# Kernel tuning notes

Hardware: AMD Instinct MI355X
Metric: run time of the kernel (lower is better)

Reference implementation:

```python
import jax, jax.numpy as jnp
import numpy as np

N_NODES = 50000
N_EDGES = 600000
N_PAIRS = 200000
D_IN, D_HID = 128, 256


def _sage_conv(x, src, dst, W_l, b_l, W_r, num_nodes):
    # PyG SAGEConv('mean'): out = mean_agg(x_j) @ W_l + b_l + x @ W_r
    msgs = x[src]                                              # [E, d] gather
    agg = jax.ops.segment_sum(msgs, dst, num_segments=num_nodes)
    deg = jax.ops.segment_sum(jnp.ones((src.shape[0],), x.dtype), dst,
                              num_segments=num_nodes)
    agg = agg / jnp.maximum(deg, 1.0)[:, None]                 # mean, safe for deg=0
    return agg @ W_l + b_l + x @ W_r


def setup_inputs() -> dict:
    key = jax.random.key(0)
    ks = jax.random.split(key, 8)
    s = lambda d: 1.0 / np.sqrt(d)
    return {
        "features": jax.random.normal(ks[0], (N_NODES, D_IN), jnp.float32),
        "edge_index": jax.random.randint(ks[1], (2, N_EDGES), 0, N_NODES, jnp.int64),
        "mask": jax.random.randint(ks[2], (N_PAIRS, 2), 0, N_NODES, jnp.int64),
        "W1l": jax.random.normal(ks[3], (D_IN, D_HID), jnp.float32) * s(D_IN),
        "b1l": jnp.zeros((D_HID,), jnp.float32),
        "W1r": jax.random.normal(ks[4], (D_IN, D_HID), jnp.float32) * s(D_IN),
        "W2l": jax.random.normal(ks[5], (D_HID, D_IN), jnp.float32) * s(D_HID),
        "b2l": jnp.zeros((D_IN,), jnp.float32),
        "W2r": jax.random.normal(ks[6], (D_HID, D_IN), jnp.float32) * s(D_HID),
        "Wlin": jax.random.normal(ks[7], (2 * D_IN, 1), jnp.float32) * s(2 * D_IN),
        "blin": jnp.zeros((1,), jnp.float32),
    }


def reference(features, edge_index, mask, W1l, b1l, W1r, W2l, b2l, W2r, Wlin, blin):
    n = features.shape[0]
    src, dst = edge_index[0], edge_index[1]
    h = _sage_conv(features, src, dst, W1l, b1l, W1r, n)       # [N, 256]
    h = jax.nn.relu(h)                                         # dropout p=0 -> identity
    h = _sage_conv(h, src, dst, W2l, b2l, W2r, n)              # [N, 128]
    m = mask.T                                                 # [2, P]
    p1 = jax.lax.stop_gradient(h[m[0]])                        # detach in original
    p2 = jax.lax.stop_gradient(h[m[1]])
    pair = jnp.concatenate((p1, p2), axis=1)                   # [P, 256]
    return jax.nn.sigmoid(pair @ Wlin + blin)                  # [P, 1]
```

## Files before the change

kernel.cpp:

```cpp
#include <hip/hip_runtime.h>
#include <math.h>

#define NN 50000
#define NE 600000
#define NP 200000
#define NB_SCAN 49

typedef unsigned int uint;
typedef unsigned short ushort;
typedef __attribute__((ext_vector_type(8))) short bf16x8;
typedef __attribute__((ext_vector_type(4))) float f32x4;

__device__ __forceinline__ ushort f2bf(float f) {
    uint u = __float_as_uint(f);
    uint r = (u + 0x7FFFu + ((u >> 16) & 1u)) >> 16;
    return (ushort)r;
}
__device__ __forceinline__ float bf2f(uint lo16) {
    return __uint_as_float(lo16 << 16);
}

__device__ __forceinline__ int wave_iscan(int v, int lane) {
#pragma unroll
    for (int off = 1; off < 64; off <<= 1) {
        int t = __shfl_up(v, off, 64);
        if (lane >= off) v += t;
    }
    return v;
}

template <int K, int N>
__device__ __forceinline__ void prepB_one(int idx, const float* __restrict__ Wt,
                                          const float* __restrict__ Wb,
                                          ushort* __restrict__ Bp) {
    int lane = idx & 63;
    int nt = (idx >> 6) % (N / 16);
    int ct = idx / (64 * (N / 16));
    int n = nt * 16 + (lane & 15);
    int kb = ct * 32 + (lane >> 4) * 8;
#pragma unroll
    for (int j = 0; j < 8; j++) {
        int k = kb + j;
        float w = (k < K / 2) ? Wt[(size_t)k * N + n] : Wb[(size_t)(k - K / 2) * N + n];
        Bp[(size_t)idx * 8 + j] = f2bf(w);
    }
}

#define T_PREP (NN * 32)
#define T_DEG  (T_PREP + NE)
#define T_B1   (T_DEG + 8192)
#define T_PQ   (T_B1 + 1024)
#define T_CAB  (T_PQ + 2)
__global__ void k_pre(const float* __restrict__ x, uint* __restrict__ A1u,
                      const int* __restrict__ dst, int* __restrict__ deg,
                      const float* __restrict__ W1l, const float* __restrict__ W1r,
                      ushort* __restrict__ Bp1,
                      const float* __restrict__ W2l, const float* __restrict__ W2r,
                      const float* __restrict__ Wlin, const float* __restrict__ b2l,
                      float* __restrict__ pq, float* __restrict__ cab) {
    int t = blockIdx.x * 256 + threadIdx.x;
    if (t < T_PREP) {
        int n = t >> 5, c4 = t & 31;
        float4 v = *(const float4*)(x + (size_t)n * 128 + c4 * 4);
        uint2 o;
        o.x = (uint)f2bf(v.x) | ((uint)f2bf(v.y) << 16);
        o.y = (uint)f2bf(v.z) | ((uint)f2bf(v.w) << 16);
        *(uint2*)(A1u + (size_t)n * 128 + 64 + c4 * 2) = o;
    } else if (t < T_DEG) {
        atomicAdd(deg + dst[t - T_PREP], 1);
    } else if (t < T_B1) {
        prepB_one<256, 256>(t - T_DEG, W1l, W1r, Bp1);
    } else if (t < T_PQ) {
        int idx = t - T_B1;
        int vec = idx >> 8;
        int k = idx & 255;
        const float* W = (vec < 2) ? W2l : W2r;
        const float* wl = Wlin + (vec & 1) * 128;
        float s = 0.f;
#pragma unroll 4
        for (int j = 0; j < 128; j++) s += W[(size_t)k * 128 + j] * wl[j];
        pq[idx] = s;
    } else if (t < T_CAB) {
        int i = t - T_PQ;
        float s = 0.f;
        for (int j = 0; j < 128; j++) s += b2l[j] * Wlin[i * 128 + j];
        cab[i] = s;
    }
}

__global__ __launch_bounds__(1024) void k_scan1(const int* __restrict__ deg,
                                                int* __restrict__ excl,
                                                int* __restrict__ bsum) {
    int tid = threadIdx.x;
    int i = blockIdx.x * 1024 + tid;
    int lane = tid & 63, wid = tid >> 6;
    int v = (i < NN) ? deg[i] : 0;
    int incl = wave_iscan(v, lane);
    __shared__ int wt[16];
    if (lane == 63) wt[wid] = incl;
    __syncthreads();
    if (tid < 16) {
        int w = wt[tid];
#pragma unroll
        for (int off = 1; off < 16; off <<= 1) {
            int t = __shfl_up(w, off, 64);
            if (tid >= off) w += t;
        }
        wt[tid] = w;
    }
    __syncthreads();
    int base = (wid > 0) ? wt[wid - 1] : 0;
    if (i < NN) excl[i] = incl - v + base;
    if (tid == 0) bsum[blockIdx.x] = wt[15];
}

__global__ __launch_bounds__(1024) void k_scan23(const int* __restrict__ excl,
                                                 const int* __restrict__ bsum,
                                                 int* __restrict__ rowptr,
                                                 int* __restrict__ cursor) {
    __shared__ int boff;
    int tid = threadIdx.x;
    if (tid < 64) {
        int v = (tid < NB_SCAN) ? bsum[tid] : 0;
        int incl = wave_iscan(v, tid);
        if (tid == (int)blockIdx.x) boff = incl - v;
    }
    __syncthreads();
    int i = blockIdx.x * 1024 + tid;
    if (i < NN) {
        int v = excl[i] + boff;
        rowptr[i] = v;
        cursor[i] = v;
    }
    if (i == 0) rowptr[NN] = NE;
}

__global__ void k_fill(const int* __restrict__ src, const int* __restrict__ dst,
                       int* __restrict__ cursor, int* __restrict__ ssrc) {
    int e = blockIdx.x * 256 + threadIdx.x;
    if (e >= NE) return;
    int d = dst[e];
    int pos = atomicAdd(cursor + d, 1);
    ssrc[pos] = src[e];
}

__global__ void k_agg1(uint* __restrict__ A1u, const int* __restrict__ rowptr,
                       const int* __restrict__ ssrc) {
    int t = blockIdx.x * 256 + threadIdx.x;
    int n = t >> 6;
    if (n >= NN) return;
    int lane = t & 63;
    int g = lane >> 4;
    int s = lane & 15;
    int r0 = rowptr[n], r1 = rowptr[n + 1];
    float a0[8] = {0.f, 0.f, 0.f, 0.f, 0.f, 0.f, 0.f, 0.f};
    float a1[8] = {0.f, 0.f, 0.f, 0.f, 0.f, 0.f, 0.f, 0.f};
    int e = r0;
    for (; e + 8 <= r1; e += 8) {
        int sA = ssrc[e + g];
        int sB = ssrc[e + 4 + g];
        uint4 vA = *(const uint4*)(A1u + (size_t)sA * 128 + 64 + s * 4);
        uint4 vB = *(const uint4*)(A1u + (size_t)sB * 128 + 64 + s * 4);
        a0[0] += bf2f(vA.x & 0xffffu); a0[1] += bf2f(vA.x >> 16);
        a0[2] += bf2f(vA.y & 0xffffu); a0[3] += bf2f(vA.y >> 16);
        a0[4] += bf2f(vA.z & 0xffffu); a0[5] += bf2f(vA.z >> 16);
        a0[6] += bf2f(vA.w & 0xffffu); a0[7] += bf2f(vA.w >> 16);
        a1[0] += bf2f(vB.x & 0xffffu); a1[1] += bf2f(vB.x >> 16);
        a1[2] += bf2f(vB.y & 0xffffu); a1[3] += bf2f(vB.y >> 16);
        a1[4] += bf2f(vB.z & 0xffffu); a1[5] += bf2f(vB.z >> 16);
        a1[6] += bf2f(vB.w & 0xffffu); a1[7] += bf2f(vB.w >> 16);
    }
    if (e + 4 <= r1) {
        int sA = ssrc[e + g];
        uint4 vA = *(const uint4*)(A1u + (size_t)sA * 128 + 64 + s * 4);
        a0[0] += bf2f(vA.x & 0xffffu); a0[1] += bf2f(vA.x >> 16);
        a0[2] += bf2f(vA.y & 0xffffu); a0[3] += bf2f(vA.y >> 16);
        a0[4] += bf2f(vA.z & 0xffffu); a0[5] += bf2f(vA.z >> 16);
        a0[6] += bf2f(vA.w & 0xffffu); a0[7] += bf2f(vA.w >> 16);
        e += 4;
    }
    int rem = r1 - e;
    if (g < rem) {
        int sB = ssrc[e + g];
        uint4 vB = *(const uint4*)(A1u + (size_t)sB * 128 + 64 + s * 4);
        a1[0] += bf2f(vB.x & 0xffffu); a1[1] += bf2f(vB.x >> 16);
        a1[2] += bf2f(vB.y & 0xffffu); a1[3] += bf2f(vB.y >> 16);
        a1[4] += bf2f(vB.z & 0xffffu); a1[5] += bf2f(vB.z >> 16);
        a1[6] += bf2f(vB.w & 0xffffu); a1[7] += bf2f(vB.w >> 16);
    }
    float ax[8];
#pragma unroll
    for (int j = 0; j < 8; j++) ax[j] = a0[j] + a1[j];
#pragma unroll
    for (int j = 0; j < 8; j++) {
        ax[j] += __shfl_xor(ax[j], 16, 64);
        ax[j] += __shfl_xor(ax[j], 32, 64);
    }
    if (g == 0) {
        float sc = 1.0f / fmaxf((float)(r1 - r0), 1.0f);
        uint4 o;
        o.x = (uint)f2bf(ax[0] * sc) | ((uint)f2bf(ax[1] * sc) << 16);
        o.y = (uint)f2bf(ax[2] * sc) | ((uint)f2bf(ax[3] * sc) << 16);
        o.z = (uint)f2bf(ax[4] * sc) | ((uint)f2bf(ax[5] * sc) << 16);
        o.w = (uint)f2bf(ax[6] * sc) | ((uint)f2bf(ax[7] * sc) << 16);
        *(uint4*)(A1u + (size_t)n * 128 + s * 4) = o;
    }
}

__global__ __launch_bounds__(256) void k_gemm1(const ushort* __restrict__ A,
                                               const ushort* __restrict__ Bp,
                                               const float* __restrict__ bias,
                                               const float* __restrict__ pq,
                                               float2* __restrict__ g2,
                                               float2* __restrict__ u2) {
    const int K = 256, NTW = 4;
    int wave = threadIdx.x >> 6;
    int lane = threadIdx.x & 63;
    int quad = lane >> 4;
    int l15 = lane & 15;
    int mbase = blockIdx.x * 32;
    int r0 = mbase + l15;       if (r0 >= NN) r0 = NN - 1;
    int r1 = mbase + 16 + l15;  if (r1 >= NN) r1 = NN - 1;
    f32x4 acc0[NTW], acc1[NTW];
#pragma unroll
    for (int i = 0; i < NTW; i++) {
        acc0[i] = (f32x4){0.f, 0.f, 0.f, 0.f};
        acc1[i] = (f32x4){0.f, 0.f, 0.f, 0.f};
    }
    const bf16x8* bp = (const bf16x8*)Bp;
#pragma unroll
    for (int ct = 0; ct < K / 32; ct++) {
        bf16x8 a0 = *(const bf16x8*)(A + (size_t)r0 * K + ct * 32 + quad * 8);
        bf16x8 a1 = *(const bf16x8*)(A + (size_t)r1 * K + ct * 32 + quad * 8);
#pragma unroll
        for (int ntl = 0; ntl < NTW; ntl++) {
            int nt = wave * NTW + ntl;
            bf16x8 b = bp[(ct * 16 + nt) * 64 + lane];
            acc0[ntl] = __builtin_amdgcn_mfma_f32_16x16x32_bf16(a0, b, acc0[ntl], 0, 0, 0);
            acc1[ntl] = __builtin_amdgcn_mfma_f32_16x16x32_bf16(a1, b, acc1[ntl], 0, 0, 0);
        }
    }
    float pga[2][4] = {{0,0,0,0},{0,0,0,0}}, pgb[2][4] = {{0,0,0,0},{0,0,0,0}};
    float pua[2][4] = {{0,0,0,0},{0,0,0,0}}, pub[2][4] = {{0,0,0,0},{0,0,0,0}};
#pragma unroll
    for (int ntl = 0; ntl < NTW; ntl++) {
        int col = (wave * NTW + ntl) * 16 + l15;
        float bv = bias[col];
        float wpa = pq[col], wpb = pq[256 + col];
        float wqa = pq[512 + col], wqb = pq[768 + col];
#pragma unroll
        for (int reg = 0; reg < 4; reg++) {
            float v0 = acc0[ntl][reg] + bv;  v0 = v0 > 0.f ? v0 : 0.f;
            float v1 = acc1[ntl][reg] + bv;  v1 = v1 > 0.f ? v1 : 0.f;
            pga[0][reg] += v0 * wpa;  pgb[0][reg] += v0 * wpb;
            pua[0][reg] += v0 * wqa;  pub[0][reg] += v0 * wqb;
            pga[1][reg] += v1 * wpa;  pgb[1][reg] += v1 * wpb;
            pua[1][reg] += v1 * wqa;  pub[1][reg] += v1 * wqb;
        }
    }
#pragma unroll
    for (int off = 1; off < 16; off <<= 1) {
#pragma unroll
        for (int rt = 0; rt < 2; rt++) {
#pragma unroll
            for (int reg = 0; reg < 4; reg++) {
                pga[rt][reg] += __shfl_xor(pga[rt][reg], off, 64);
                pgb[rt][reg] += __shfl_xor(pgb[rt][reg], off, 64);
                pua[rt][reg] += __shfl_xor(pua[rt][reg], off, 64);
                pub[rt][reg] += __shfl_xor(pub[rt][reg], off, 64);
            }
        }
    }
    __shared__ float red[4][4][32];
    if (l15 == 0) {
#pragma unroll
        for (int rt = 0; rt < 2; rt++) {
#pragma unroll
            for (int reg = 0; reg < 4; reg++) {
                int row = rt * 16 + quad * 4 + reg;
                red[0][wave][row] = pga[rt][reg];
                red[1][wave][row] = pgb[rt][reg];
                red[2][wave][row] = pua[rt][reg];
                red[3][wave][row] = pub[rt][reg];
            }
        }
    }
    __syncthreads();
    if (threadIdx.x < 32) {
        int row = threadIdx.x;
        int m = mbase + row;
        if (m < NN) {
            float ga = (red[0][0][row] + red[0][1][row]) + (red[0][2][row] + red[0][3][row]);
            float gb = (red[1][0][row] + red[1][1][row]) + (red[1][2][row] + red[1][3][row]);
            float ua = (red[2][0][row] + red[2][1][row]) + (red[2][2][row] + red[2][3][row]);
            float ub = (red[3][0][row] + red[3][1][row]) + (red[3][2][row] + red[3][3][row]);
            g2[m] = make_float2(ga, gb);
            u2[m] = make_float2(ua, ub);
        }
    }
}

__global__ void k_sagg(const float2* __restrict__ g2, const float2* __restrict__ u2,
                       const int* __restrict__ rowptr, const int* __restrict__ ssrc,
                       const float* __restrict__ cab,
                       float* __restrict__ sa, float* __restrict__ sb) {
    int n = blockIdx.x * 256 + threadIdx.x;
    if (n >= NN) return;
    int r0 = rowptr[n], r1 = rowptr[n + 1];
    float a0 = 0.f, b0 = 0.f, a1 = 0.f, b1 = 0.f;
    float a2 = 0.f, b2 = 0.f, a3 = 0.f, b3 = 0.f;
    int e = r0;
    for (; e + 4 <= r1; e += 4) {
        float2 v0 = g2[ssrc[e]];
        float2 v1 = g2[ssrc[e + 1]];
        float2 v2 = g2[ssrc[e + 2]];
        float2 v3 = g2[ssrc[e + 3]];
        a0 += v0.x; b0 += v0.y;
        a1 += v1.x; b1 += v1.y;
        a2 += v2.x; b2 += v2.y;
        a3 += v3.x; b3 += v3.y;
    }
    for (; e < r1; e++) {
        float2 v = g2[ssrc[e]];
        a0 += v.x; b0 += v.y;
    }
    float sc = 1.0f / fmaxf((float)(r1 - r0), 1.0f);
    float2 u = u2[n];
    sa[n] = ((a0 + a1) + (a2 + a3)) * sc + u.x + cab[0];
    sb[n] = ((b0 + b1) + (b2 + b3)) * sc + u.y + cab[1];
}

__global__ void k_pairs(const float* __restrict__ sa, const float* __restrict__ sb,
                        const int* __restrict__ mask, const float* __restrict__ blin,
                        float* __restrict__ out) {
    int p = blockIdx.x * 256 + threadIdx.x;
    if (p >= NP) return;
    int2 m = ((const int2*)mask)[p];
    float v = sa[m.x] + sb[m.y] + blin[0];
    out[p] = 1.0f / (1.0f + __expf(-v));
}

extern "C" void kernel_launch(void* const* d_in, const int* in_sizes, int n_in,
                              void* d_out, int out_size, void* d_ws, size_t ws_size,
                              hipStream_t stream) {
    const float* x    = (const float*)d_in[0];
    const int*   ei   = (const int*)  d_in[1];
    const int*   mask = (const int*)  d_in[2];
    const float* W1l  = (const float*)d_in[3];
    const float* b1l  = (const float*)d_in[4];
    const float* W1r  = (const float*)d_in[5];
    const float* W2l  = (const float*)d_in[6];
    const float* b2l  = (const float*)d_in[7];
    const float* W2r  = (const float*)d_in[8];
    const float* Wlin = (const float*)d_in[9];
    const float* blin = (const float*)d_in[10];
    float* out = (float*)d_out;

    const int* src = ei;
    const int* dst = ei + NE;

    char* ws = (char*)d_ws;
    int*    deg    = (int*)(ws);
    int*    rowptr = (int*)(ws + (size_t)1 * (1 << 20));
    int*    cursor = (int*)(ws + (size_t)2 * (1 << 20));
    int*    ssrc   = (int*)(ws + (size_t)3 * (1 << 20));
    int*    excl   = (int*)(ws + (size_t)6 * (1 << 20));
    int*    bsum   = (int*)(ws + (size_t)7 * (1 << 20));
    ushort* Bp1    = (ushort*)(ws + (size_t)8 * (1 << 20));
    float*  pq     = (float*)(ws + (size_t)9 * (1 << 20));
    float*  cab    = (float*)(ws + (size_t)9 * (1 << 20) + 65536);
    float*  sa     = (float*)(ws + (size_t)10 * (1 << 20));
    float*  sb     = (float*)(ws + (size_t)11 * (1 << 20));
    float2* g2     = (float2*)(ws + (size_t)12 * (1 << 20));
    float2* u2     = (float2*)(ws + (size_t)13 * (1 << 20));
    uint*   A1u    = (uint*)(ws + (size_t)14 * (1 << 20));

    hipMemsetAsync(deg, 0, (size_t)NN * 4, stream);

    k_pre   <<<(T_CAB + 255) / 256, 256, 0, stream>>>(x, A1u, dst, deg,
                                                      W1l, W1r, Bp1,
                                                      W2l, W2r, Wlin, b2l, pq, cab);
    k_scan1 <<<NB_SCAN, 1024, 0, stream>>>(deg, excl, bsum);
    k_scan23<<<NB_SCAN, 1024, 0, stream>>>(excl, bsum, rowptr, cursor);
    k_fill  <<<(NE + 255) / 256, 256, 0, stream>>>(src, dst, cursor, ssrc);

    k_agg1  <<<NN / 4, 256, 0, stream>>>(A1u, rowptr, ssrc);
    k_gemm1 <<<(NN + 31) / 32, 256, 0, stream>>>((const ushort*)A1u, Bp1, b1l,
                                                 pq, g2, u2);
    k_sagg  <<<(NN + 255) / 256, 256, 0, stream>>>(g2, u2, rowptr, ssrc, cab, sa, sb);
    k_pairs <<<(NP + 255) / 256, 256, 0, stream>>>(sa, sb, mask, blin, out);
}
```

Before: 218.3 us.

## Fuse scan and CSR fill with grid barriers; fuse aggregation into GEMM via LDS

Merges the two scan kernels and the fill kernel into a single 49-block kernel that uses atomic-flag grid barriers, relying on all 49 blocks being co-resident. It also fuses the layer-1 mean aggregation into the GEMM kernel: each block aggregates its 32 rows and stages them together with the self features in LDS, so the concatenated activation matrix is no longer written to and re-read from global memory. This removes kernel launches and an intermediate buffer round trip. The cost is a fill phase running on only 49 blocks with less parallelism, and GEMM blocks that now carry serial gather latency before any MFMA work starts.

```diff
diff --git a/kernel.cpp b/kernel.cpp
--- a/kernel.cpp
+++ b/kernel.cpp
@@ -51,7 +51,7 @@
 #define T_B1   (T_DEG + 8192)
 #define T_PQ   (T_B1 + 1024)
 #define T_CAB  (T_PQ + 2)
-__global__ void k_pre(const float* __restrict__ x, uint* __restrict__ A1u,
+__global__ void k_pre(const float* __restrict__ x, uint* __restrict__ xb,
                       const int* __restrict__ dst, int* __restrict__ deg,
                       const float* __restrict__ W1l, const float* __restrict__ W1r,
                       ushort* __restrict__ Bp1,
@@ -65,7 +65,7 @@
         uint2 o;
         o.x = (uint)f2bf(v.x) | ((uint)f2bf(v.y) << 16);
         o.y = (uint)f2bf(v.z) | ((uint)f2bf(v.w) << 16);
-        *(uint2*)(A1u + (size_t)n * 128 + 64 + c4 * 2) = o;
+        *(uint2*)(xb + (size_t)n * 64 + c4 * 2) = o;
     } else if (t < T_DEG) {
         atomicAdd(deg + dst[t - T_PREP], 1);
     } else if (t < T_B1) {
@@ -88,15 +88,21 @@
     }
 }
 
-__global__ __launch_bounds__(1024) void k_scan1(const int* __restrict__ deg,
-                                                int* __restrict__ excl,
-                                                int* __restrict__ bsum) {
+__global__ __launch_bounds__(1024) void k_scanfill(const int* __restrict__ deg,
+                                                   int* __restrict__ bsum,
+                                                   int* __restrict__ flags,
+                                                   int* __restrict__ rowptr,
+                                                   int* __restrict__ cursor,
+                                                   const int* __restrict__ src,
+                                                   const int* __restrict__ dst,
+                                                   int* __restrict__ ssrc) {
     int tid = threadIdx.x;
     int i = blockIdx.x * 1024 + tid;
     int lane = tid & 63, wid = tid >> 6;
     int v = (i < NN) ? deg[i] : 0;
     int incl = wave_iscan(v, lane);
     __shared__ int wt[16];
+    __shared__ int sboff;
     if (lane == 63) wt[wid] = incl;
     __syncthreads();
     if (tid < 16) {
@@ -110,117 +116,151 @@
     }
     __syncthreads();
     int base = (wid > 0) ? wt[wid - 1] : 0;
-    if (i < NN) excl[i] = incl - v + base;
-    if (tid == 0) bsum[blockIdx.x] = wt[15];
-}
-
-__global__ __launch_bounds__(1024) void k_scan23(const int* __restrict__ excl,
-                                                 const int* __restrict__ bsum,
-                                                 int* __restrict__ rowptr,
-                                                 int* __restrict__ cursor) {
-    __shared__ int boff;
+    int excl_local = incl - v + base;
+    if (tid == 0)
+        __hip_atomic_store(&bsum[blockIdx.x], wt[15], __ATOMIC_RELEASE,
+                           __HIP_MEMORY_SCOPE_AGENT);
+    __syncthreads();
+    if (tid == 0) {
+        __hip_atomic_fetch_add(&flags[0], 1, __ATOMIC_ACQ_REL, __HIP_MEMORY_SCOPE_AGENT);
+        while (__hip_atomic_load(&flags[0], __ATOMIC_ACQUIRE,
+                                 __HIP_MEMORY_SCOPE_AGENT) < NB_SCAN) {}
+    }
+    __syncthreads();
+    if (tid < 64) {
+        int b = (tid < NB_SCAN && tid < (int)blockIdx.x)
+                    ? __hip_atomic_load(&bsum[tid], __ATOMIC_ACQUIRE,
+                                        __HIP_MEMORY_SCOPE_AGENT)
+                    : 0;
+#pragma unroll
+        for (int off = 1; off < 64; off <<= 1) b += __shfl_xor(b, off, 64);
+        if (tid == 0) sboff = b;
+    }
+    __syncthreads();
+    int boff = sboff;
+    if (i < NN) {
+        int rv = excl_local + boff;
+        rowptr[i] = rv;
+        __hip_atomic_store(&cursor[i], rv, __ATOMIC_RELAXED, __HIP_MEMORY_SCOPE_AGENT);
+    }
+    if (i == 0) rowptr[NN] = NE;
+    __syncthreads();
+    if (tid == 0) {
+        __hip_atomic_fetch_add(&flags[1], 1, __ATOMIC_ACQ_REL, __HIP_MEMORY_SCOPE_AGENT);
+        while (__hip_atomic_load(&flags[1], __ATOMIC_ACQUIRE,
+                                 __HIP_MEMORY_SCOPE_AGENT) < NB_SCAN) {}
+    }
+    __syncthreads();
+    const int STRIDE = NB_SCAN * 4096;
+    for (int e0 = blockIdx.x * 4096 + tid * 4; e0 < NE; e0 += STRIDE) {
+        int4 d4 = *(const int4*)(dst + e0);
+        int4 s4 = *(const int4*)(src + e0);
+        int p0 = __hip_atomic_fetch_add(&cursor[d4.x], 1, __ATOMIC_RELAXED,
+                                        __HIP_MEMORY_SCOPE_AGENT);
+        int p1 = __hip_atomic_fetch_add(&cursor[d4.y], 1, __ATOMIC_RELAXED,
+                                        __HIP_MEMORY_SCOPE_AGENT);
+        int p2 = __hip_atomic_fetch_add(&cursor[d4.z], 1, __ATOMIC_RELAXED,
+                                        __HIP_MEMORY_SCOPE_AGENT);
+        int p3 = __hip_atomic_fetch_add(&cursor[d4.w], 1, __ATOMIC_RELAXED,
+                                        __HIP_MEMORY_SCOPE_AGENT);
+        ssrc[p0] = s4.x;
+        ssrc[p1] = s4.y;
+        ssrc[p2] = s4.z;
+        ssrc[p3] = s4.w;
+    }
+}
+
+#define LDSROW 264
+__global__ __launch_bounds__(256) void k_agg_gemm(const uint* __restrict__ xb,
+                                                  const ushort* __restrict__ Bp,
+                                                  const int* __restrict__ rowptr,
+                                                  const int* __restrict__ ssrc,
+                                                  const float* __restrict__ bias,
+                                                  const float* __restrict__ pq,
+                                                  float2* __restrict__ g2,
+                                                  float2* __restrict__ u2) {
+    __shared__ ushort At[32][LDSROW];
+    __shared__ float red[4][4][32];
+    const int NTW = 4;
     int tid = threadIdx.x;
-    if (tid < 64) {
-        int v = (tid < NB_SCAN) ? bsum[tid] : 0;
-        int incl = wave_iscan(v, tid);
-        if (tid == (int)blockIdx.x) boff = incl - v;
-    }
-    __syncthreads();
-    int i = blockIdx.x * 1024 + tid;
-    if (i < NN) {
-        int v = excl[i] + boff;
-        rowptr[i] = v;
-        cursor[i] = v;
-    }
-    if (i == 0) rowptr[NN] = NE;
-}
-
-__global__ void k_fill(const int* __restrict__ src, const int* __restrict__ dst,
-                       int* __restrict__ cursor, int* __restrict__ ssrc) {
-    int e = blockIdx.x * 256 + threadIdx.x;
-    if (e >= NE) return;
-    int d = dst[e];
-    int pos = atomicAdd(cursor + d, 1);
-    ssrc[pos] = src[e];
-}
-
-__global__ void k_agg1(uint* __restrict__ A1u, const int* __restrict__ rowptr,
-                       const int* __restrict__ ssrc) {
-    int t = blockIdx.x * 256 + threadIdx.x;
-    int n = t >> 6;
-    if (n >= NN) return;
-    int lane = t & 63;
-    int g = lane >> 4;
-    int s = lane & 15;
-    int r0 = rowptr[n], r1 = rowptr[n + 1];
-    float a0[8] = {0.f, 0.f, 0.f, 0.f, 0.f, 0.f, 0.f, 0.f};
-    float a1[8] = {0.f, 0.f, 0.f, 0.f, 0.f, 0.f, 0.f, 0.f};
-    int e = r0;
-    for (; e + 8 <= r1; e += 8) {
-        int sA = ssrc[e + g];
-        int sB = ssrc[e + 4 + g];
-        uint4 vA = *(const uint4*)(A1u + (size_t)sA * 128 + 64 + s * 4);
-        uint4 vB = *(const uint4*)(A1u + (size_t)sB * 128 + 64 + s * 4);
-        a0[0] += bf2f(vA.x & 0xffffu); a0[1] += bf2f(vA.x >> 16);
-        a0[2] += bf2f(vA.y & 0xffffu); a0[3] += bf2f(vA.y >> 16);
-        a0[4] += bf2f(vA.z & 0xffffu); a0[5] += bf2f(vA.z >> 16);
-        a0[6] += bf2f(vA.w & 0xffffu); a0[7] += bf2f(vA.w >> 16);
-        a1[0] += bf2f(vB.x & 0xffffu); a1[1] += bf2f(vB.x >> 16);
-        a1[2] += bf2f(vB.y & 0xffffu); a1[3] += bf2f(vB.y >> 16);
-        a1[4] += bf2f(vB.z & 0xffffu); a1[5] += bf2f(vB.z >> 16);
-        a1[6] += bf2f(vB.w & 0xffffu); a1[7] += bf2f(vB.w >> 16);
-    }
-    if (e + 4 <= r1) {
-        int sA = ssrc[e + g];
-        uint4 vA = *(const uint4*)(A1u + (size_t)sA * 128 + 64 + s * 4);
-        a0[0] += bf2f(vA.x & 0xffffu); a0[1] += bf2f(vA.x >> 16);
-        a0[2] += bf2f(vA.y & 0xffffu); a0[3] += bf2f(vA.y >> 16);
-        a0[4] += bf2f(vA.z & 0xffffu); a0[5] += bf2f(vA.z >> 16);
-        a0[6] += bf2f(vA.w & 0xffffu); a0[7] += bf2f(vA.w >> 16);
-        e += 4;
-    }
-    int rem = r1 - e;
-    if (g < rem) {
-        int sB = ssrc[e + g];
-        uint4 vB = *(const uint4*)(A1u + (size_t)sB * 128 + 64 + s * 4);
-        a1[0] += bf2f(vB.x & 0xffffu); a1[1] += bf2f(vB.x >> 16);
-        a1[2] += bf2f(vB.y & 0xffffu); a1[3] += bf2f(vB.y >> 16);
-        a1[4] += bf2f(vB.z & 0xffffu); a1[5] += bf2f(vB.z >> 16);
-        a1[6] += bf2f(vB.w & 0xffffu); a1[7] += bf2f(vB.w >> 16);
-    }
-    float ax[8];
-#pragma unroll
-    for (int j = 0; j < 8; j++) ax[j] = a0[j] + a1[j];
-#pragma unroll
-    for (int j = 0; j < 8; j++) {
-        ax[j] += __shfl_xor(ax[j], 16, 64);
-        ax[j] += __shfl_xor(ax[j], 32, 64);
-    }
-    if (g == 0) {
-        float sc = 1.0f / fmaxf((float)(r1 - r0), 1.0f);
-        uint4 o;
-        o.x = (uint)f2bf(ax[0] * sc) | ((uint)f2bf(ax[1] * sc) << 16);
-        o.y = (uint)f2bf(ax[2] * sc) | ((uint)f2bf(ax[3] * sc) << 16);
-        o.z = (uint)f2bf(ax[4] * sc) | ((uint)f2bf(ax[5] * sc) << 16);
-        o.w = (uint)f2bf(ax[6] * sc) | ((uint)f2bf(ax[7] * sc) << 16);
-        *(uint4*)(A1u + (size_t)n * 128 + s * 4) = o;
-    }
-}
-
-__global__ __launch_bounds__(256) void k_gemm1(const ushort* __restrict__ A,
-                                               const ushort* __restrict__ Bp,
-                                               const float* __restrict__ bias,
-                                               const float* __restrict__ pq,
-                                               float2* __restrict__ g2,
-                                               float2* __restrict__ u2) {
-    const int K = 256, NTW = 4;
-    int wave = threadIdx.x >> 6;
-    int lane = threadIdx.x & 63;
-    int quad = lane >> 4;
-    int l15 = lane & 15;
+    int wave = tid >> 6, lane = tid & 63;
+    int g = lane >> 4, s = lane & 15;
     int mbase = blockIdx.x * 32;
-    int r0 = mbase + l15;       if (r0 >= NN) r0 = NN - 1;
-    int r1 = mbase + 16 + l15;  if (r1 >= NN) r1 = NN - 1;
+
+#pragma unroll
+    for (int it = 0; it < 2; it++) {
+        int idx = it * 256 + tid;
+        int row = idx >> 4, c = idx & 15;
+        int node = mbase + row;
+        if (node >= NN) node = NN - 1;
+        uint4 v = *(const uint4*)(xb + (size_t)node * 64 + c * 4);
+        *(uint4*)(&At[row][128 + c * 8]) = v;
+    }
+
+    for (int q = 0; q < 8; q++) {
+        int tr = wave * 8 + q;
+        int n = mbase + tr;
+        if (n < NN) {
+            int r0 = rowptr[n], r1 = rowptr[n + 1];
+            float a0[8] = {0.f, 0.f, 0.f, 0.f, 0.f, 0.f, 0.f, 0.f};
+            float a1[8] = {0.f, 0.f, 0.f, 0.f, 0.f, 0.f, 0.f, 0.f};
+            int e = r0;
+            for (; e + 8 <= r1; e += 8) {
+                int sA = ssrc[e + g];
+                int sB = ssrc[e + 4 + g];
+                uint4 vA = *(const uint4*)(xb + (size_t)sA * 64 + s * 4);
+                uint4 vB = *(const uint4*)(xb + (size_t)sB * 64 + s * 4);
+                a0[0] += bf2f(vA.x & 0xffffu); a0[1] += bf2f(vA.x >> 16);
+                a0[2] += bf2f(vA.y & 0xffffu); a0[3] += bf2f(vA.y >> 16);
+                a0[4] += bf2f(vA.z & 0xffffu); a0[5] += bf2f(vA.z >> 16);
+                a0[6] += bf2f(vA.w & 0xffffu); a0[7] += bf2f(vA.w >> 16);
+                a1[0] += bf2f(vB.x & 0xffffu); a1[1] += bf2f(vB.x >> 16);
+                a1[2] += bf2f(vB.y & 0xffffu); a1[3] += bf2f(vB.y >> 16);
+                a1[4] += bf2f(vB.z & 0xffffu); a1[5] += bf2f(vB.z >> 16);
+                a1[6] += bf2f(vB.w & 0xffffu); a1[7] += bf2f(vB.w >> 16);
+            }
+            if (e + 4 <= r1) {
+                int sA = ssrc[e + g];
+                uint4 vA = *(const uint4*)(xb + (size_t)sA * 64 + s * 4);
+                a0[0] += bf2f(vA.x & 0xffffu); a0[1] += bf2f(vA.x >> 16);
+                a0[2] += bf2f(vA.y & 0xffffu); a0[3] += bf2f(vA.y >> 16);
+                a0[4] += bf2f(vA.z & 0xffffu); a0[5] += bf2f(vA.z >> 16);
+                a0[6] += bf2f(vA.w & 0xffffu); a0[7] += bf2f(vA.w >> 16);
+                e += 4;
+            }
+            int rem = r1 - e;
+            if (g < rem) {
+                int sB = ssrc[e + g];
+                uint4 vB = *(const uint4*)(xb + (size_t)sB * 64 + s * 4);
+                a1[0] += bf2f(vB.x & 0xffffu); a1[1] += bf2f(vB.x >> 16);
+                a1[2] += bf2f(vB.y & 0xffffu); a1[3] += bf2f(vB.y >> 16);
+                a1[4] += bf2f(vB.z & 0xffffu); a1[5] += bf2f(vB.z >> 16);
+                a1[6] += bf2f(vB.w & 0xffffu); a1[7] += bf2f(vB.w >> 16);
+            }
+            float ax[8];
+#pragma unroll
+            for (int j = 0; j < 8; j++) ax[j] = a0[j] + a1[j];
+#pragma unroll
+            for (int j = 0; j < 8; j++) {
+                ax[j] += __shfl_xor(ax[j], 16, 64);
+                ax[j] += __shfl_xor(ax[j], 32, 64);
+            }
+            if (g == 0) {
+                float sc = 1.0f / fmaxf((float)(r1 - r0), 1.0f);
+                uint4 o;
+                o.x = (uint)f2bf(ax[0] * sc) | ((uint)f2bf(ax[1] * sc) << 16);
+                o.y = (uint)f2bf(ax[2] * sc) | ((uint)f2bf(ax[3] * sc) << 16);
+                o.z = (uint)f2bf(ax[4] * sc) | ((uint)f2bf(ax[5] * sc) << 16);
+                o.w = (uint)f2bf(ax[6] * sc) | ((uint)f2bf(ax[7] * sc) << 16);
+                *(uint4*)(&At[tr][s * 8]) = o;
+            }
+        } else if (g == 0) {
+            *(uint4*)(&At[tr][s * 8]) = make_uint4(0, 0, 0, 0);
+        }
+    }
+    __syncthreads();
+
+    int quad = lane >> 4, l15 = lane & 15;
     f32x4 acc0[NTW], acc1[NTW];
 #pragma unroll
     for (int i = 0; i < NTW; i++) {
@@ -229,9 +269,9 @@
     }
     const bf16x8* bp = (const bf16x8*)Bp;
 #pragma unroll
-    for (int ct = 0; ct < K / 32; ct++) {
-        bf16x8 a0 = *(const bf16x8*)(A + (size_t)r0 * K + ct * 32 + quad * 8);
-        bf16x8 a1 = *(const bf16x8*)(A + (size_t)r1 * K + ct * 32 + quad * 8);
+    for (int ct = 0; ct < 8; ct++) {
+        bf16x8 a0 = *(const bf16x8*)(&At[l15][ct * 32 + quad * 8]);
+        bf16x8 a1 = *(const bf16x8*)(&At[16 + l15][ct * 32 + quad * 8]);
 #pragma unroll
         for (int ntl = 0; ntl < NTW; ntl++) {
             int nt = wave * NTW + ntl;
@@ -271,7 +311,6 @@
             }
         }
     }
-    __shared__ float red[4][4][32];
     if (l15 == 0) {
 #pragma unroll
         for (int rt = 0; rt < 2; rt++) {
@@ -361,11 +400,11 @@
 
     char* ws = (char*)d_ws;
     int*    deg    = (int*)(ws);
+    int*    flags  = (int*)(ws + 0xF0000);
     int*    rowptr = (int*)(ws + (size_t)1 * (1 << 20));
     int*    cursor = (int*)(ws + (size_t)2 * (1 << 20));
     int*    ssrc   = (int*)(ws + (size_t)3 * (1 << 20));
-    int*    excl   = (int*)(ws + (size_t)6 * (1 << 20));
-    int*    bsum   = (int*)(ws + (size_t)7 * (1 << 20));
+    int*    bsum   = (int*)(ws + (size_t)6 * (1 << 20));
     ushort* Bp1    = (ushort*)(ws + (size_t)8 * (1 << 20));
     float*  pq     = (float*)(ws + (size_t)9 * (1 << 20));
     float*  cab    = (float*)(ws + (size_t)9 * (1 << 20) + 65536);
@@ -373,20 +412,17 @@
     float*  sb     = (float*)(ws + (size_t)11 * (1 << 20));
     float2* g2     = (float2*)(ws + (size_t)12 * (1 << 20));
     float2* u2     = (float2*)(ws + (size_t)13 * (1 << 20));
-    uint*   A1u    = (uint*)(ws + (size_t)14 * (1 << 20));
-
-    hipMemsetAsync(deg, 0, (size_t)NN * 4, stream);
-
-    k_pre   <<<(T_CAB + 255) / 256, 256, 0, stream>>>(x, A1u, dst, deg,
-                                                      W1l, W1r, Bp1,
-                                                      W2l, W2r, Wlin, b2l, pq, cab);
-    k_scan1 <<<NB_SCAN, 1024, 0, stream>>>(deg, excl, bsum);
-    k_scan23<<<NB_SCAN, 1024, 0, stream>>>(excl, bsum, rowptr, cursor);
-    k_fill  <<<(NE + 255) / 256, 256, 0, stream>>>(src, dst, cursor, ssrc);
-
-    k_agg1  <<<NN / 4, 256, 0, stream>>>(A1u, rowptr, ssrc);
-    k_gemm1 <<<(NN + 31) / 32, 256, 0, stream>>>((const ushort*)A1u, Bp1, b1l,
-                                                 pq, g2, u2);
-    k_sagg  <<<(NN + 255) / 256, 256, 0, stream>>>(g2, u2, rowptr, ssrc, cab, sa, sb);
-    k_pairs <<<(NP + 255) / 256, 256, 0, stream>>>(sa, sb, mask, blin, out);
-}
+    uint*   xb     = (uint*)(ws + (size_t)14 * (1 << 20));
+
+    hipMemsetAsync(ws, 0, (size_t)1 << 20, stream);
+
+    k_pre     <<<(T_CAB + 255) / 256, 256, 0, stream>>>(x, xb, dst, deg,
+                                                        W1l, W1r, Bp1,
+                                                        W2l, W2r, Wlin, b2l, pq, cab);
+    k_scanfill<<<NB_SCAN, 1024, 0, stream>>>(deg, bsum, flags, rowptr, cursor,
+                                             src, dst, ssrc);
+    k_agg_gemm<<<(NN + 31) / 32, 256, 0, stream>>>(xb, Bp1, rowptr, ssrc, b1l,
+                                                   pq, g2, u2);
+    k_sagg    <<<(NN + 255) / 256, 256, 0, stream>>>(g2, u2, rowptr, ssrc, cab, sa, sb);
+    k_pairs   <<<(NP + 255) / 256, 256, 0, stream>>>(sa, sb, mask, blin, out);
+}
```

After: 244.3 us. 1.12x slower.
